# Optimization experiments

Measured on AMD Instinct MI355X. Metric: run time of the kernel, lower is better.

Reference implementation:

```python
import jax, jax.numpy as jnp
import numpy as np

B, S, D, H = 2, 2048, 1024, 16
HD = D // H  # 64


def setup_inputs() -> dict:
    key = jax.random.key(0)
    ks = jax.random.split(key, 10)
    inp = {
        "queries": jax.random.normal(ks[0], (B, S, D), dtype=jnp.float32),
        "keys": jax.random.normal(ks[1], (B, S, D), dtype=jnp.float32),
        "values": jax.random.normal(ks[2], (B, S, D), dtype=jnp.float32),
        "attention_mask": jax.random.randint(ks[3], (B, S), 0, 2, dtype=jnp.int32),
        # Linear params (torch nn.Linear: y = x @ W.T + b), scaled like default init
        "Wq": jax.random.normal(ks[4], (D, D), dtype=jnp.float32) / np.sqrt(D),
        "bq": jnp.zeros((D,), dtype=jnp.float32),
        "Wk": jax.random.normal(ks[5], (D, D), dtype=jnp.float32) / np.sqrt(D),
        "bk": jnp.zeros((D,), dtype=jnp.float32),
        "Wv": jax.random.normal(ks[6], (D, D), dtype=jnp.float32) / np.sqrt(D),
        "bv": jnp.zeros((D,), dtype=jnp.float32),
    }
    return inp


def _split_heads(x):
    # torch.chunk along last dim + stack(dim=1) == reshape + transpose
    b, s, d = x.shape
    return x.reshape(b, s, H, HD).transpose(0, 2, 1, 3)  # [B,H,S,hd]


def reference(queries, keys, values, attention_mask, Wq, bq, Wk, bk, Wv, bv):
    q = jax.nn.relu(queries @ Wq.T + bq)
    k = jax.nn.relu(keys @ Wk.T + bk)
    v = jax.nn.relu(values @ Wv.T + bv)
    qh, kh, vh = _split_heads(q), _split_heads(k), _split_heads(v)
    score = jnp.einsum("bhqd,bhkd->bhqk", qh, kh) / jnp.sqrt(jnp.float32(HD))
    # enc mask: [B,1,S,1] broadcast over key dim — masks whole query rows where mask==0
    row_mask = (attention_mask == 0)[:, None, :, None]
    score = jnp.where(row_mask, jnp.float32(-1e9), score)
    attn = jax.nn.softmax(score, axis=-1)
    a = jnp.einsum("bhqk,bhkd->bhqd", attn, vh)  # [B,H,S,hd]
    # faithful to original: permute(0,1,3,2) then reshape to (B,S,D)
    a = a.transpose(0, 1, 3, 2).reshape(q.shape[0], q.shape[1], q.shape[2])
    return a + queries
```

## Files before the change

### kernel.cpp

```cpp
#include <hip/hip_runtime.h>
#include <hip/hip_bf16.h>

#define DEV __device__ __forceinline__

typedef __attribute__((ext_vector_type(8))) short short8;
typedef __attribute__((ext_vector_type(4))) float f32x4;

#define MFMA16(a, b, c) __builtin_amdgcn_mfma_f32_16x16x32_bf16((a), (b), (c), 0, 0, 0)

static constexpr int B_ = 2, S_ = 2048, D_ = 1024, H_ = 16, HD_ = 64;
static constexpr long NX = (long)B_ * S_ * D_;
static constexpr long NW = (long)D_ * D_;

DEV short f2bf(float f) {
    __hip_bfloat16 h = __float2bfloat16(f);
    union { __hip_bfloat16 hh; short s; } u;
    u.hh = h;
    return u.s;
}

DEV float bf2f(short s) {
    union { float f; unsigned u; } x;
    x.u = ((unsigned)(unsigned short)s) << 16;
    return x.f;
}

DEV unsigned cvtpk(float a, float b) {
    unsigned r;
    asm("v_cvt_pk_bf16_f32 %0, %1, %2" : "=v"(r) : "v"(a), "v"(b));
    return r;
}

DEV short8 pk8(float4 lo, float4 hi) {
    union { short8 s8; unsigned u[4]; } u;
    u.u[0] = cvtpk(lo.x, lo.y);
    u.u[1] = cvtpk(lo.z, lo.w);
    u.u[2] = cvtpk(hi.x, hi.y);
    u.u[3] = cvtpk(hi.z, hi.w);
    return u.s8;
}

DEV short8 ld8(const short* p) { return *(const short8*)p; }

DEV void gld16(const short* g, short* l) {
    __builtin_amdgcn_global_load_lds(
        (const __attribute__((address_space(1))) unsigned int*)g,
        (__attribute__((address_space(3))) unsigned int*)l, 16, 0, 0);
}

__global__ __launch_bounds__(256) void convert_w(
    const float* __restrict__ wq, const float* __restrict__ wk, const float* __restrict__ wv,
    short* __restrict__ wqb, short* __restrict__ wkb, short* __restrict__ wvb) {
    long tid = (long)blockIdx.x * 256 + threadIdx.x;
    long e = tid * 4;
    const float* src; short* dst; long off;
    if      (e < NW)     { src = wq; dst = wqb; off = e; }
    else if (e < 2*NW)   { src = wk; dst = wkb; off = e - NW; }
    else                 { src = wv; dst = wvb; off = e - 2*NW; }
    float4 f = *(const float4*)(src + off);
    short4 o;
    o.x = f2bf(f.x); o.y = f2bf(f.y); o.z = f2bf(f.z); o.w = f2bf(f.w);
    *(short4*)(dst + off) = o;
}

__global__ __launch_bounds__(256) void gemm_bias_relu(
    const float* __restrict__ X0, const float* __restrict__ X1, const float* __restrict__ X2,
    const short* __restrict__ W0, const short* __restrict__ W1, const short* __restrict__ W2,
    const float* __restrict__ b0, const float* __restrict__ b1, const float* __restrict__ b2,
    short* __restrict__ O0, short* __restrict__ O1, short* __restrict__ O2) {
    __shared__ short As[2][128 * 32];
    __shared__ short Bs[2][128 * 32];

    const int bid = blockIdx.x;
    const int tl  = (bid & 7) * 96 + (bid >> 3);
    const int bx  = tl & 7;
    const int by  = (tl >> 3) & 31;
    const int z   = tl >> 8;

    const float* X   = (z == 0) ? X0 : (z == 1) ? X1 : X2;
    const short* W   = (z == 0) ? W0 : (z == 1) ? W1 : W2;
    const float* bia = (z == 0) ? b0 : (z == 1) ? b1 : b2;
    short*       Out = (z == 0) ? O0 : (z == 1) ? O1 : O2;

    const int tid  = threadIdx.x;
    const int wid  = tid >> 6;
    const int lane = tid & 63;
    const int id   = lane & 15;
    const int quad = lane >> 4;
    const int m0 = by * 128;
    const int n0 = bx * 128;
    const int wm = (wid >> 1) * 64;
    const int wn = (wid & 1) * 64;

    const float* Ag  = X + (long)(m0 + wid * 32 + (lane >> 2)) * D_ + (lane & 3) * 8;
    const short* Bg0 = W + (long)(n0 + wid * 32 + (lane >> 2)) * D_ + (lane & 3) * 8;
    const int offW = wid * 1024;
    const int aDst = offW + lane * 8;

    f32x4 acc[4][4] = {};

#define COMPUTE(cur)                                                              \
    do {                                                                          \
        short8 af[4], bf[4];                                                      \
        _Pragma("unroll")                                                         \
        for (int i = 0; i < 4; i++)                                               \
            af[i] = ld8(&As[cur][(wm + 16*i + id) * 32 + quad * 8]);              \
        _Pragma("unroll")                                                         \
        for (int j = 0; j < 4; j++)                                               \
            bf[j] = ld8(&Bs[cur][(wn + 16*j + id) * 32 + quad * 8]);              \
        _Pragma("unroll")                                                         \
        for (int i = 0; i < 4; i++)                                               \
            _Pragma("unroll")                                                     \
            for (int j = 0; j < 4; j++)                                           \
                acc[i][j] = MFMA16(af[i], bf[j], acc[i][j]);                      \
    } while (0)

    float4 ae0 = *(const float4*)(Ag);
    float4 ae1 = *(const float4*)(Ag + 4);
    float4 ae2 = *(const float4*)(Ag + 16 * D_);
    float4 ae3 = *(const float4*)(Ag + 16 * D_ + 4);
    float4 ao0 = *(const float4*)(Ag + 32);
    float4 ao1 = *(const float4*)(Ag + 36);
    float4 ao2 = *(const float4*)(Ag + 16 * D_ + 32);
    float4 ao3 = *(const float4*)(Ag + 16 * D_ + 36);
    gld16(Bg0,            &Bs[0][offW]);
    gld16(Bg0 + 16 * D_,  &Bs[0][offW + 512]);
    *(short8*)(&As[0][aDst])       = pk8(ae0, ae1);
    *(short8*)(&As[0][aDst + 512]) = pk8(ae2, ae3);

    for (int t = 0; t < 32; t += 2) {
        const int kkO = t * 32 + 32;
        __syncthreads();
        gld16(Bg0 + kkO,            &Bs[1][offW]);
        gld16(Bg0 + 16 * D_ + kkO,  &Bs[1][offW + 512]);
        COMPUTE(0);
        *(short8*)(&As[1][aDst])       = pk8(ao0, ao1);
        *(short8*)(&As[1][aDst + 512]) = pk8(ao2, ao3);
        if (t + 2 < 32) {
            ae0 = *(const float4*)(Ag + kkO + 32);
            ae1 = *(const float4*)(Ag + kkO + 36);
            ae2 = *(const float4*)(Ag + 16 * D_ + kkO + 32);
            ae3 = *(const float4*)(Ag + 16 * D_ + kkO + 36);
        }
        __syncthreads();
        if (t + 2 < 32) {
            gld16(Bg0 + kkO + 32,            &Bs[0][offW]);
            gld16(Bg0 + 16 * D_ + kkO + 32,  &Bs[0][offW + 512]);
        }
        COMPUTE(1);
        if (t + 2 < 32) {
            *(short8*)(&As[0][aDst])       = pk8(ae0, ae1);
            *(short8*)(&As[0][aDst + 512]) = pk8(ae2, ae3);
        }
        if (t + 3 < 32) {
            ao0 = *(const float4*)(Ag + kkO + 64);
            ao1 = *(const float4*)(Ag + kkO + 68);
            ao2 = *(const float4*)(Ag + 16 * D_ + kkO + 64);
            ao3 = *(const float4*)(Ag + 16 * D_ + kkO + 68);
        }
    }
#undef COMPUTE

#pragma unroll
    for (int j = 0; j < 4; j++) {
        int col = n0 + wn + 16*j + id;
        float bj = bia[col];
#pragma unroll
        for (int i = 0; i < 4; i++) {
#pragma unroll
            for (int r = 0; r < 4; r++) {
                int row = m0 + wm + 16*i + quad*4 + r;
                float val = fmaxf(acc[i][j][r] + bj, 0.f);
                Out[(long)row * D_ + col] = f2bf(val);
            }
        }
    }
}

__global__ __launch_bounds__(256) void transpose_v(const short* __restrict__ Vp,
                                                   short* __restrict__ VT) {
    __shared__ short tile[64 * 64];
    const int bh = blockIdx.y;
    const int b = bh >> 4, h = bh & 15;
    const int s0 = blockIdx.x * 64;
    const int t = threadIdx.x;
#pragma unroll
    for (int it = 0; it < 2; it++) {
        int row = (t >> 3) + 32 * it;
        int u   = t & 7;
        short8 d = ld8(Vp + (long)(b * S_ + s0 + row) * D_ + h * HD_ + u * 8);
        *(short8*)(&tile[row * 64 + (u ^ ((row >> 3) & 7)) * 8]) = d;
    }
    __syncthreads();
#pragma unroll
    for (int it = 0; it < 2; it++) {
        int e  = (t >> 3) + 32 * it;
        int sb = (t & 7) * 8;
        short8 o;
#pragma unroll
        for (int u = 0; u < 8; u++) {
            int row = sb + u;
            o[u] = tile[row * 64 + (((e >> 3) ^ ((row >> 3) & 7)) * 8) + (e & 7)];
        }
        *(short8*)(VT + ((long)bh * HD_ + e) * S_ + s0 + sb) = o;
    }
}

__global__ __launch_bounds__(256, 2) void attention(
    const short* __restrict__ Qb, const short* __restrict__ Kb,
    const short* __restrict__ VT, const int* __restrict__ mask,
    const float* __restrict__ queries, float* __restrict__ out) {
    __shared__ short Ks[2][64 * 64];
    __shared__ short Vs[2][64 * 64];
    __shared__ short pl[4][2 * 16 * 72];

    const int tid  = threadIdx.x;
    const int wid  = tid >> 6;
    const int lane = tid & 63;
    const int id   = lane & 15;
    const int quad = lane >> 4;

    const int bid = blockIdx.x;
    const int w   = bid >> 3;
    const int bh  = (bid & 7) + 8 * (w & 3);
    const int qt  = w >> 2;
    const int b   = bh >> 4;
    const int h   = bh & 15;
    const int q0  = qt * 128 + wid * 32;

    short8 qf[2][2];
#pragma unroll
    for (int g = 0; g < 2; g++) {
        const short* qbase = Qb + (long)(b * S_ + q0 + g * 16 + id) * D_ + h * HD_ + quad * 8;
        short8 f0 = ld8(qbase);
        short8 f1 = ld8(qbase + 32);
        const float qsc = mask[b * S_ + q0 + g * 16 + id] ? 0.125f : 0.f;
#pragma unroll
        for (int i = 0; i < 8; i++) {
            f0[i] = f2bf(bf2f(f0[i]) * qsc);
            f1[i] = f2bf(bf2f(f1[i]) * qsc);
        }
        qf[g][0] = f0; qf[g][1] = f1;
    }

    const int srow = wid * 16 + (lane >> 3);
    const int su   = (lane & 7) ^ (srow & 7);
    const short* kg0 = Kb + ((long)b * S_ + srow) * D_ + h * HD_ + su * 8;
    const short* vg0 = VT + (((long)(b * H_ + h) * HD_) + srow) * S_ + su * 8;
    short* plw = pl[wid];

    const int swz = id & 7;

    float l4[2][4] = {};
    f32x4 o[2][4] = {};

    gld16(kg0,            &Ks[0][wid * 1024]);
    gld16(kg0 + 8 * D_,   &Ks[0][wid * 1024 + 512]);
    gld16(vg0,            &Vs[0][wid * 1024]);
    gld16(vg0 + 8 * S_,   &Vs[0][wid * 1024 + 512]);

    for (int c0 = 0; c0 < S_; c0 += 64) {
        const int cur = (c0 >> 6) & 1;
        __syncthreads();
        if (c0 + 64 < S_) {
            const int nxt = cur ^ 1;
            const long cg = (long)(c0 + 64);
            gld16(kg0 + cg * D_,           &Ks[nxt][wid * 1024]);
            gld16(kg0 + cg * D_ + 8 * D_,  &Ks[nxt][wid * 1024 + 512]);
            gld16(vg0 + cg,                &Vs[nxt][wid * 1024]);
            gld16(vg0 + cg + 8 * S_,       &Vs[nxt][wid * 1024 + 512]);
        }

        f32x4 s[2][4];
#pragma unroll
        for (int g = 0; g < 2; g++)
#pragma unroll
            for (int t = 0; t < 4; t++) s[g][t] = (f32x4){0.f, 0.f, 0.f, 0.f};
#pragma unroll
        for (int t = 0; t < 4; t++) {
            short8 a0 = ld8(&Ks[cur][(16*t + id) * 64 + ((quad    ) ^ swz) * 8]);
            short8 a1 = ld8(&Ks[cur][(16*t + id) * 64 + ((quad ^ 4) ^ swz) * 8]);
            s[0][t] = MFMA16(a0, qf[0][0], s[0][t]);
            s[0][t] = MFMA16(a1, qf[0][1], s[0][t]);
            s[1][t] = MFMA16(a0, qf[1][0], s[1][t]);
            s[1][t] = MFMA16(a1, qf[1][1], s[1][t]);
        }

#pragma unroll
        for (int g = 0; g < 2; g++) {
            short* plg = plw + g * (16 * 72);
#pragma unroll
            for (int t = 0; t < 4; t++) {
                float p0 = __expf(s[g][t][0]);
                float p1 = __expf(s[g][t][1]);
                float p2 = __expf(s[g][t][2]);
                float p3 = __expf(s[g][t][3]);
                l4[g][0] += p0; l4[g][1] += p1; l4[g][2] += p2; l4[g][3] += p3;
                uint2 w2;
                w2.x = cvtpk(p0, p1);
                w2.y = cvtpk(p2, p3);
                *(uint2*)(&plg[id * 72 + 16 * t + quad * 4]) = w2;
            }
        }
        short8 pf[2][2];
#pragma unroll
        for (int g = 0; g < 2; g++) {
            short* plg = plw + g * (16 * 72);
            pf[g][0] = ld8(&plg[id * 72 + quad * 8]);
            pf[g][1] = ld8(&plg[id * 72 + 32 + quad * 8]);
        }

#pragma unroll
        for (int j2 = 0; j2 < 4; j2++) {
#pragma unroll
            for (int kh = 0; kh < 2; kh++) {
                short8 va = ld8(&Vs[cur][(16*j2 + id) * 64 + (((kh << 2) + quad) ^ swz) * 8]);
                o[0][j2] = MFMA16(va, pf[0][kh], o[0][j2]);
                o[1][j2] = MFMA16(va, pf[1][kh], o[1][j2]);
            }
        }
    }

    const long obase = (long)b * (S_ * D_) + (long)h * (HD_ * S_);
#pragma unroll
    for (int g = 0; g < 2; g++) {
        float l = l4[g][0] + l4[g][1] + l4[g][2] + l4[g][3];
        l += __shfl_xor(l, 16);
        l += __shfl_xor(l, 32);
        const float linv = 1.f / l;
#pragma unroll
        for (int j2 = 0; j2 < 4; j2++) {
#pragma unroll
            for (int r = 0; r < 4; r++) {
                int dim = 16 * j2 + quad * 4 + r;
                long idx = obase + (long)dim * S_ + q0 + g * 16 + id;
                out[idx] = o[g][j2][r] * linv + queries[idx];
            }
        }
    }
}

extern "C" void kernel_launch(void* const* d_in, const int* in_sizes, int n_in,
                              void* d_out, int out_size, void* d_ws, size_t ws_size,
                              hipStream_t stream) {
    const float* queries = (const float*)d_in[0];
    const float* keys    = (const float*)d_in[1];
    const float* values  = (const float*)d_in[2];
    const int*   mask    = (const int*)d_in[3];
    const float* Wq = (const float*)d_in[4];
    const float* bq = (const float*)d_in[5];
    const float* Wk = (const float*)d_in[6];
    const float* bk = (const float*)d_in[7];
    const float* Wv = (const float*)d_in[8];
    const float* bv = (const float*)d_in[9];
    float* out = (float*)d_out;

    short* ws  = (short*)d_ws;
    short* wqb = ws;
    short* wkb = wqb + NW;
    short* wvb = wkb + NW;
    short* Q   = wvb + NW;
    short* K   = Q   + NX;
    short* Vp  = K   + NX;
    short* VT  = Vp  + NX;

    convert_w<<<3072, 256, 0, stream>>>(Wq, Wk, Wv, wqb, wkb, wvb);
    gemm_bias_relu<<<768, 256, 0, stream>>>(queries, keys, values, wqb, wkb, wvb,
                                            bq, bk, bv, Q, K, Vp);
    transpose_v<<<dim3(32, 32), 256, 0, stream>>>(Vp, VT);
    attention<<<512, 256, 0, stream>>>(Q, K, VT, mask, queries, out);
}
```

Measured before the change: 224.7 us.

## Reschedule projection GEMM pipeline with explicit waitcnt fences instead of syncthreads

Reorders the double-buffered main loop of the QKV projection GEMM. Each stage now writes the next A tile to LDS and issues the B global-to-LDS loads and the following A register loads before its MFMA compute. It replaces __syncthreads with a hand-written s_waitcnt vmcnt(N)/lgkmcnt(0) plus s_barrier and sched_barrier. With vmcnt(4), only the LDS-bound B loads must finish at each barrier, while the four A register loads stay in flight across it, so memory latency can hide behind compute. The cost is fragile manual counter bookkeeping: a wrong count or an unexpected compiler reordering could cause a race.

```diff
diff --git a/kernel.cpp b/kernel.cpp
--- a/kernel.cpp
+++ b/kernel.cpp
@@ -42,7 +42,7 @@
 
 DEV short8 ld8(const short* p) { return *(const short8*)p; }
 
-DEV void gld16(const short* g, short* l) {
+DEV void gld16(const void* g, void* l) {
     __builtin_amdgcn_global_load_lds(
         (const __attribute__((address_space(1))) unsigned int*)g,
         (__attribute__((address_space(3))) unsigned int*)l, 16, 0, 0);
@@ -98,6 +98,20 @@
     const int aDst = offW + lane * 8;
 
     f32x4 acc[4][4] = {};
+
+#define ALOAD(dst0, dst1, dst2, dst3, kk_)                  \
+    do {                                                    \
+        dst0 = *(const float4*)(Ag + (kk_));                \
+        dst1 = *(const float4*)(Ag + (kk_) + 4);            \
+        dst2 = *(const float4*)(Ag + (kk_) + 16 * D_);      \
+        dst3 = *(const float4*)(Ag + (kk_) + 16 * D_ + 4);  \
+    } while (0)
+
+#define AWRITE(buf, s0, s1, s2, s3)                          \
+    do {                                                     \
+        *(short8*)(&As[buf][aDst])       = pk8(s0, s1);      \
+        *(short8*)(&As[buf][aDst + 512]) = pk8(s2, s3);      \
+    } while (0)
 
 #define COMPUTE(cur)                                                              \
     do {                                                                          \
@@ -115,51 +129,46 @@
                 acc[i][j] = MFMA16(af[i], bf[j], acc[i][j]);                      \
     } while (0)
 
-    float4 ae0 = *(const float4*)(Ag);
-    float4 ae1 = *(const float4*)(Ag + 4);
-    float4 ae2 = *(const float4*)(Ag + 16 * D_);
-    float4 ae3 = *(const float4*)(Ag + 16 * D_ + 4);
-    float4 ao0 = *(const float4*)(Ag + 32);
-    float4 ao1 = *(const float4*)(Ag + 36);
-    float4 ao2 = *(const float4*)(Ag + 16 * D_ + 32);
-    float4 ao3 = *(const float4*)(Ag + 16 * D_ + 36);
+#define FENCE(vm)                                                         \
+    do {                                                                  \
+        asm volatile("s_waitcnt vmcnt(" #vm ") lgkmcnt(0)" ::: "memory"); \
+        __builtin_amdgcn_s_barrier();                                     \
+        __builtin_amdgcn_sched_barrier(0);                                \
+    } while (0)
+
+    float4 ae0, ae1, ae2, ae3;
+    float4 ao0, ao1, ao2, ao3;
+
     gld16(Bg0,            &Bs[0][offW]);
     gld16(Bg0 + 16 * D_,  &Bs[0][offW + 512]);
-    *(short8*)(&As[0][aDst])       = pk8(ae0, ae1);
-    *(short8*)(&As[0][aDst + 512]) = pk8(ae2, ae3);
+    ALOAD(ae0, ae1, ae2, ae3, 0);
+    ALOAD(ao0, ao1, ao2, ao3, 32);
+    AWRITE(0, ae0, ae1, ae2, ae3);
+    asm volatile("s_waitcnt lgkmcnt(0)" ::: "memory");
+    __builtin_amdgcn_s_barrier();
+    __builtin_amdgcn_sched_barrier(0);
 
     for (int t = 0; t < 32; t += 2) {
-        const int kkO = t * 32 + 32;
-        __syncthreads();
-        gld16(Bg0 + kkO,            &Bs[1][offW]);
-        gld16(Bg0 + 16 * D_ + kkO,  &Bs[1][offW + 512]);
+        const int kk1 = t * 32 + 32;
+        AWRITE(1, ao0, ao1, ao2, ao3);
+        gld16(Bg0 + kk1,            &Bs[1][offW]);
+        gld16(Bg0 + kk1 + 16 * D_,  &Bs[1][offW + 512]);
+        if (t + 2 < 32) ALOAD(ae0, ae1, ae2, ae3, kk1 + 32);
         COMPUTE(0);
-        *(short8*)(&As[1][aDst])       = pk8(ao0, ao1);
-        *(short8*)(&As[1][aDst + 512]) = pk8(ao2, ao3);
+        if (t + 2 < 32) FENCE(4); else FENCE(0);
         if (t + 2 < 32) {
-            ae0 = *(const float4*)(Ag + kkO + 32);
-            ae1 = *(const float4*)(Ag + kkO + 36);
-            ae2 = *(const float4*)(Ag + 16 * D_ + kkO + 32);
-            ae3 = *(const float4*)(Ag + 16 * D_ + kkO + 36);
-        }
-        __syncthreads();
-        if (t + 2 < 32) {
-            gld16(Bg0 + kkO + 32,            &Bs[0][offW]);
-            gld16(Bg0 + 16 * D_ + kkO + 32,  &Bs[0][offW + 512]);
+            AWRITE(0, ae0, ae1, ae2, ae3);
+            gld16(Bg0 + kk1 + 32,            &Bs[0][offW]);
+            gld16(Bg0 + kk1 + 32 + 16 * D_,  &Bs[0][offW + 512]);
+            if (t + 3 < 32) ALOAD(ao0, ao1, ao2, ao3, kk1 + 64);
         }
         COMPUTE(1);
-        if (t + 2 < 32) {
-            *(short8*)(&As[0][aDst])       = pk8(ae0, ae1);
-            *(short8*)(&As[0][aDst + 512]) = pk8(ae2, ae3);
-        }
-        if (t + 3 < 32) {
-            ao0 = *(const float4*)(Ag + kkO + 64);
-            ao1 = *(const float4*)(Ag + kkO + 68);
-            ao2 = *(const float4*)(Ag + 16 * D_ + kkO + 64);
-            ao3 = *(const float4*)(Ag + 16 * D_ + kkO + 68);
-        }
-    }
+        if (t + 2 < 32) { if (t + 3 < 32) FENCE(4); else FENCE(0); }
+    }
+#undef ALOAD
+#undef AWRITE
 #undef COMPUTE
+#undef FENCE
 
 #pragma unroll
     for (int j = 0; j < 4; j++) {
```

Result: slower. 230.2 us (+2.4%).
